# Optimization experiments

Hardware: AMD Instinct MI355X
Metric: run time of the kernel (lower is better)

Reference implementation:

```python
import jax, jax.numpy as jnp
import numpy as np

H = 128          # hidden_dim
EPS = 1e-5       # BatchNorm eps


def _mean_aggr(h_src, src_idx, dst_idx, num_dst):
    # scatter-mean of h_src rows (gathered by src_idx) onto dst nodes
    msgs = h_src[src_idx]                                   # [E, H] gather
    s = jax.ops.segment_sum(msgs, dst_idx, num_segments=num_dst)
    c = jax.ops.segment_sum(jnp.ones((dst_idx.shape[0],), h_src.dtype),
                            dst_idx, num_segments=num_dst)
    return s / jnp.maximum(c, 1.0)[:, None]


def _bn_eval(h, g, b, m, v):
    return (h - m) * jax.lax.rsqrt(v + EPS) * g + b


def setup_inputs() -> dict:
    key = jax.random.key(0)
    ks = jax.random.split(key, 32)
    Nu, Nr, E, Din, ED = 100000, 100000, 500000, 32, 16
    d = {}
    d['x_user'] = jax.random.normal(ks[0], (Nu, Din), jnp.float32)
    d['x_recipient'] = jax.random.normal(ks[1], (Nr, Din), jnp.float32)
    d['edge_attr'] = jax.random.normal(ks[2], (E, ED), jnp.float32)
    d['edge_index_ut'] = jax.random.randint(ks[3], (2, E), 0, Nr)  # user->recipient
    d['edge_index_ru'] = jax.random.randint(ks[4], (2, E), 0, Nu)  # recipient->user
    sc = 0.05
    # input projections (Linear: y = x @ W + b, W stored [in, out])
    d['proj_uW'] = jax.random.normal(ks[5], (Din, H), jnp.float32) * sc
    d['proj_ub'] = jnp.zeros((H,), jnp.float32)
    d['proj_rW'] = jax.random.normal(ks[6], (Din, H), jnp.float32) * sc
    d['proj_rb'] = jnp.zeros((H,), jnp.float32)
    # SAGEConv params: [num_layers=2, num_edge_types=2, ...]
    d['sage_Wl'] = jax.random.normal(ks[7], (2, 2, H, H), jnp.float32) * sc
    d['sage_bl'] = jnp.zeros((2, 2, H), jnp.float32)
    d['sage_Wr'] = jax.random.normal(ks[8], (2, 2, H, H), jnp.float32) * sc
    # BatchNorm (eval): [num_layers=2, num_node_types=2 (0=user,1=recipient), H]
    d['bn_g'] = jnp.ones((2, 2, H), jnp.float32)
    d['bn_b'] = jnp.zeros((2, 2, H), jnp.float32)
    d['bn_m'] = jax.random.normal(ks[9], (2, 2, H), jnp.float32) * 0.01
    d['bn_v'] = jnp.ones((2, 2, H), jnp.float32)
    # EdgePredictor MLP: (2H + edge_dim) -> H -> H//2 -> 1
    din = 2 * H + ED
    d['ep_W1'] = jax.random.normal(ks[10], (din, H), jnp.float32) * sc
    d['ep_b1'] = jnp.zeros((H,), jnp.float32)
    d['ep_bng'] = jnp.ones((H,), jnp.float32)
    d['ep_bnb'] = jnp.zeros((H,), jnp.float32)
    d['ep_bnm'] = jax.random.normal(ks[11], (H,), jnp.float32) * 0.01
    d['ep_bnv'] = jnp.ones((H,), jnp.float32)
    d['ep_W2'] = jax.random.normal(ks[12], (H, H // 2), jnp.float32) * sc
    d['ep_b2'] = jnp.zeros((H // 2,), jnp.float32)
    d['ep_W3'] = jax.random.normal(ks[13], (H // 2, 1), jnp.float32) * sc
    d['ep_b3'] = jnp.zeros((1,), jnp.float32)
    return d


def reference(x_user, x_recipient, edge_attr, edge_index_ut, edge_index_ru,
              proj_uW, proj_ub, proj_rW, proj_rb,
              sage_Wl, sage_bl, sage_Wr,
              bn_g, bn_b, bn_m, bn_v,
              ep_W1, ep_b1, ep_bng, ep_bnb, ep_bnm, ep_bnv,
              ep_W2, ep_b2, ep_W3, ep_b3):
    Nu = x_user.shape[0]
    Nr = x_recipient.shape[0]
    # input projections
    h_u = x_user @ proj_uW + proj_ub        # [Nu, H]
    h_r = x_recipient @ proj_rW + proj_rb   # [Nr, H]

    for i in range(2):  # num_layers
        # edge type 0: user -> recipient (SAGE mean aggr + root)
        agg_r = _mean_aggr(h_u, edge_index_ut[0], edge_index_ut[1], Nr)
        new_r = agg_r @ sage_Wl[i, 0] + sage_bl[i, 0] + h_r @ sage_Wr[i, 0]
        # edge type 1: recipient -> user
        agg_u = _mean_aggr(h_r, edge_index_ru[0], edge_index_ru[1], Nu)
        new_u = agg_u @ sage_Wl[i, 1] + sage_bl[i, 1] + h_u @ sage_Wr[i, 1]
        # BN (eval) + ReLU (dropout inactive) + residual
        new_u = jax.nn.relu(_bn_eval(new_u, bn_g[i, 0], bn_b[i, 0], bn_m[i, 0], bn_v[i, 0])) + h_u
        new_r = jax.nn.relu(_bn_eval(new_r, bn_g[i, 1], bn_b[i, 1], bn_m[i, 1], bn_v[i, 1])) + h_r
        h_u, h_r = new_u, new_r

    # edge predictor on target edge type (user -> recipient)
    src = h_u[edge_index_ut[0]]   # [E, H]
    dst = h_r[edge_index_ut[1]]   # [E, H]
    x = jnp.concatenate([src, dst, edge_attr], axis=1)  # [E, 2H+ED]
    h = jax.nn.relu(x @ ep_W1 + ep_b1)
    h = _bn_eval(h, ep_bng, ep_bnb, ep_bnm, ep_bnv)
    h = jax.nn.relu(h @ ep_W2 + ep_b2)
    out = jax.nn.sigmoid(h @ ep_W3 + ep_b3)
    return out.squeeze(-1)  # [E]
```

## Files before the change

kernel.cpp:

```cpp
#include <hip/hip_runtime.h>
#include <math.h>

#define H 128
#define BN_EPS 1e-5f

typedef __attribute__((ext_vector_type(8))) short bf16x8;
typedef __attribute__((ext_vector_type(4))) float f32x4;
typedef __attribute__((ext_vector_type(2))) float f32x2;

__device__ __forceinline__ unsigned short f2bf(float f) {
    unsigned int u = __float_as_uint(f);
    u += 0x7fffu + ((u >> 16) & 1u);
    return (unsigned short)(u >> 16);
}
__device__ __forceinline__ float bf2f(unsigned short s) {
    return __uint_as_float(((unsigned int)s) << 16);
}
__device__ __forceinline__ f32x4 mfma16(bf16x8 a, bf16x8 b, f32x4 c) {
    return __builtin_amdgcn_mfma_f32_16x16x32_bf16(a, b, c, 0, 0, 0);
}
__device__ __forceinline__ unsigned char f2fp8(float f) {
    int p = __builtin_amdgcn_cvt_pk_fp8_f32(f, f, 0, false);
    return (unsigned char)(p & 0xff);
}

__device__ __forceinline__ void wfrag_one(const float* __restrict__ src,
                                          unsigned short* __restrict__ dst,
                                          int K, int N, int idx) {
    int l = idx & 63;
    int rest = idx >> 6;
    int ntn = N >> 4;
    int nt = rest % ntn;
    int kc = rest / ntn;
    int n = nt * 16 + (l & 15);
    int k0 = kc * 32 + (l >> 4) * 8;
    bf16x8 v;
    #pragma unroll
    for (int j = 0; j < 8; ++j) {
        int k = k0 + j;
        v[j] = (short)((k < K) ? f2bf(src[(size_t)k * N + n]) : 0);
    }
    *(bf16x8*)(dst + (size_t)idx * 8) = v;
}

__global__ __launch_bounds__(256)
void wfrag_all(const float* __restrict__ W1, const float* __restrict__ W2,
               const float* __restrict__ pu, const float* __restrict__ pr,
               const float* __restrict__ Wl, const float* __restrict__ Wr,
               unsigned short* __restrict__ W1f, unsigned short* __restrict__ W2f,
               unsigned short* __restrict__ puf, unsigned short* __restrict__ prf,
               unsigned short* __restrict__ sageWf) {
    int bx = blockIdx.x;
    if (bx < 26) {
        int idx = bx * 256 + threadIdx.x;
        if (idx < 4608)      wfrag_one(W1, W1f, 272, 128, idx);
        else if (idx < 5632) wfrag_one(W2, W2f, 128, 64, idx - 4608);
        else if (idx < 6144) wfrag_one(pu, puf, 32, 128, idx - 5632);
        else if (idx < 6656) wfrag_one(pr, prf, 32, 128, idx - 6144);
    } else {
        int idx = (bx - 26) * 256 + threadIdx.x;
        int seg = idx >> 11;
        int sub = idx & 2047;
        int lt = seg >> 1;
        int half = seg & 1;
        const float* src = (half ? Wr : Wl) + (size_t)lt * H * H;
        unsigned short* dst = sageWf + (size_t)lt * 32768 + half * 16384;
        wfrag_one(src, dst, 128, 128, sub);
    }
}

__device__ __forceinline__ int swz_of(int col) {
    int kc = col >> 5;
    int q = (col >> 3) & 3;
    int j = col & 7;
    return q * 32 + kc * 8 + j;
}

__global__ __launch_bounds__(256)
void proj_kernel(const float* __restrict__ xu, const float* __restrict__ xr,
                 const unsigned short* __restrict__ puf, const float* __restrict__ bu,
                 const unsigned short* __restrict__ prf, const float* __restrict__ br,
                 unsigned short* __restrict__ hub, unsigned short* __restrict__ hrb,
                 unsigned char* __restrict__ h8u, unsigned char* __restrict__ h8r,
                 int Nu, int Nr, int nbu) {
    int bx = blockIdx.x;
    const float* x; const unsigned short* Wf; const float* bias;
    unsigned short* hb; unsigned char* h8; int N; int row0;
    if (bx < nbu) { x = xu; Wf = puf; bias = bu; hb = hub; h8 = h8u; N = Nu; row0 = bx * 64; }
    else          { x = xr; Wf = prf; bias = br; hb = hrb; h8 = h8r; N = Nr; row0 = (bx - nbu) * 64; }

    int tid = threadIdx.x, l = tid & 63, w = tid >> 6, l15 = l & 15, quad = l >> 4;
    int arow = row0 + w * 16 + l15;

    bf16x8 a = {0, 0, 0, 0, 0, 0, 0, 0};
    if (arow < N) {
        const float* xp = x + (size_t)arow * 32 + quad * 8;
        float4 v0 = *(const float4*)xp;
        float4 v1 = *(const float4*)(xp + 4);
        a[0] = (short)f2bf(v0.x); a[1] = (short)f2bf(v0.y);
        a[2] = (short)f2bf(v0.z); a[3] = (short)f2bf(v0.w);
        a[4] = (short)f2bf(v1.x); a[5] = (short)f2bf(v1.y);
        a[6] = (short)f2bf(v1.z); a[7] = (short)f2bf(v1.w);
    }
    f32x4 acc[8];
    #pragma unroll
    for (int nt = 0; nt < 8; ++nt) {
        bf16x8 b = *(const bf16x8*)(Wf + (size_t)(nt * 64 + l) * 8);
        acc[nt] = mfma16(a, b, (f32x4){0.f, 0.f, 0.f, 0.f});
    }
    #pragma unroll
    for (int reg = 0; reg < 4; ++reg) {
        int row = row0 + w * 16 + quad * 4 + reg;
        if (row < N) {
            #pragma unroll
            for (int nt = 0; nt < 8; ++nt) {
                int col = nt * 16 + l15;
                float v = acc[nt][reg] + bias[col];
                hb[(size_t)row * H + col] = f2bf(v);
                h8[(size_t)row * H + swz_of(col)] = f2fp8(v);
            }
        }
    }
}

__global__ __launch_bounds__(256)
void hist_kernel(const int* __restrict__ dstR, const int* __restrict__ dstU,
                 int* __restrict__ degR, int* __restrict__ degU, int E, int EB) {
    int bx = blockIdx.x;
    const int* dst = (bx < EB) ? dstR : dstU;
    int* deg = (bx < EB) ? degR : degU;
    int e = ((bx < EB) ? bx : bx - EB) * 256 + threadIdx.x;
    if (e < E) atomicAdd(&deg[dst[e]], 1);
}

__global__ __launch_bounds__(256)
void scan1_kernel(const int* __restrict__ degR, const int* __restrict__ degU,
                  int* __restrict__ partR, int* __restrict__ partU, int Nr, int Nu, int NBr) {
    int bx = blockIdx.x;
    const int* deg = (bx < NBr) ? degR : degU;
    int* part = (bx < NBr) ? partR : partU;
    int lb = (bx < NBr) ? bx : bx - NBr;
    int N = (bx < NBr) ? Nr : Nu;
    __shared__ int s[256];
    int t = threadIdx.x;
    int i = lb * 256 + t;
    s[t] = (i < N) ? deg[i] : 0;
    __syncthreads();
    for (int o = 128; o > 0; o >>= 1) {
        if (t < o) s[t] += s[t + o];
        __syncthreads();
    }
    if (t == 0) part[lb] = s[0];
}

__global__ __launch_bounds__(256)
void scan3_kernel(const int* __restrict__ degR, const int* __restrict__ degU,
                  const int* __restrict__ partR, const int* __restrict__ partU,
                  int* __restrict__ offR, int* __restrict__ offU, int Nr, int Nu, int NBr) {
    int bx = blockIdx.x;
    const int* deg = (bx < NBr) ? degR : degU;
    const int* part = (bx < NBr) ? partR : partU;
    int* off = (bx < NBr) ? offR : offU;
    int lb = (bx < NBr) ? bx : bx - NBr;
    int N = (bx < NBr) ? Nr : Nu;
    __shared__ int s[256];
    __shared__ int ps[256];
    int t = threadIdx.x;

    int pv = 0;
    if (t < lb) pv += part[t];
    if (t + 256 < lb) pv += part[t + 256];
    ps[t] = pv;
    __syncthreads();
    for (int o = 128; o > 0; o >>= 1) {
        if (t < o) ps[t] += ps[t + o];
        __syncthreads();
    }
    int pref = ps[0];

    int i = lb * 256 + t;
    int v = (i < N) ? deg[i] : 0;
    s[t] = v;
    __syncthreads();
    for (int o = 1; o < 256; o <<= 1) {
        int x = (t >= o) ? s[t - o] : 0;
        __syncthreads();
        s[t] += x;
        __syncthreads();
    }
    if (i < N) off[i] = pref + s[t] - v;
    if (i == N - 1) off[N] = pref + s[t];
}

__global__ __launch_bounds__(256)
void fill_kernel(const int* __restrict__ srcR, const int* __restrict__ dstR,
                 const int* __restrict__ srcU, const int* __restrict__ dstU,
                 const int* __restrict__ offR, const int* __restrict__ offU,
                 int* __restrict__ degR, int* __restrict__ degU,
                 int* __restrict__ eidR, int* __restrict__ eidU,
                 int* __restrict__ epermR, int* __restrict__ epdstR,
                 int E, int EB) {
    int bx = blockIdx.x;
    bool isR = bx < EB;
    const int* src = isR ? srcR : srcU;
    const int* dst = isR ? dstR : dstU;
    const int* off = isR ? offR : offU;
    int* deg = isR ? degR : degU;
    int* eid = isR ? eidR : eidU;
    int e = (isR ? bx : bx - EB) * 256 + threadIdx.x;
    if (e < E) {
        int d = dst[e];
        int p = off[d] + atomicSub(&deg[d], 1) - 1;
        eid[p] = src[e];
        if (isR) {
            epermR[p] = e;
            epdstR[p] = d;
        }
    }
}

__global__ __launch_bounds__(256)
void layer_kernel(const unsigned short* __restrict__ hu_o, const unsigned short* __restrict__ hr_o,
                  const unsigned char* __restrict__ h8u_o, const unsigned char* __restrict__ h8r_o,
                  unsigned short* __restrict__ hu_n, unsigned short* __restrict__ hr_n,
                  unsigned char* __restrict__ h8u_n, unsigned char* __restrict__ h8r_n,
                  const int* __restrict__ off_r, const int* __restrict__ eid_r,
                  const int* __restrict__ off_u, const int* __restrict__ eid_u,
                  int Nu, int Nr, int nbr,
                  const unsigned short* __restrict__ WfR, const float* __restrict__ blR,
                  const float* __restrict__ gR, const float* __restrict__ bR,
                  const float* __restrict__ mR, const float* __restrict__ vR,
                  const unsigned short* __restrict__ WfU, const float* __restrict__ blU,
                  const float* __restrict__ gU, const float* __restrict__ bU,
                  const float* __restrict__ mU, const float* __restrict__ vU) {
    int bx = blockIdx.x;
    const unsigned short* own; const unsigned char* g8; unsigned short* outp; unsigned char* out8;
    const int* off; const int* eid; const unsigned short* Wf;
    const float *bl, *bg, *bb, *bm, *bv;
    int N, row0;
    if (bx < nbr) {
        g8 = h8u_o; own = hr_o; outp = hr_n; out8 = h8r_n; off = off_r; eid = eid_r;
        Wf = WfR; bl = blR; bg = gR; bb = bR; bm = mR; bv = vR;
        N = Nr; row0 = bx * 64;
    } else {
        g8 = h8r_o; own = hu_o; outp = hu_n; out8 = h8u_n; off = off_u; eid = eid_u;
        Wf = WfU; bl = blU; bg = gU; bb = bU; bm = mU; bv = vU;
        N = Nu; row0 = (bx - nbr) * 64;
    }

    __shared__ float sc[128], sh[128], bias[128];
    __shared__ int perm[64];
    int tid = threadIdx.x;
    if (tid < 128) {
        float s = bg[tid] * rsqrtf(bv[tid] + BN_EPS);
        sc[tid] = s;
        sh[tid] = bb[tid] - bm[tid] * s;
        bias[tid] = bl[tid];
    }
    if (tid < 64) {
        int rr = row0 + tid;
        int dg = (rr < N) ? (off[rr + 1] - off[rr]) : 0;
        int key = (min(dg, 255) << 8) | tid;
        for (int k = 2; k <= 64; k <<= 1) {
            for (int j = k >> 1; j > 0; j >>= 1) {
                int p = __shfl_xor(key, j);
                bool keepmin = (((tid & j) == 0) == ((tid & k) == 0));
                key = keepmin ? (key < p ? key : p) : (key > p ? key : p);
            }
        }
        perm[tid] = key & 255;
    }
    __syncthreads();

    int l = tid & 63, w = tid >> 6, l15 = l & 15, quad = l >> 4;
    int rloc = perm[w * 16 + l15];
    int arow = row0 + rloc;
    bool rok = (arow < N);
    size_t rbase = (size_t)(rok ? arow : 0) * H;
    int s0 = rok ? off[arow] : 0;
    int s1 = rok ? off[arow + 1] : 0;

    bf16x8 ownfr[4];
    #pragma unroll
    for (int kc = 0; kc < 4; ++kc)
        ownfr[kc] = *(const bf16x8*)(own + rbase + kc * 32 + quad * 8);

    float ag[4][8];
    #pragma unroll
    for (int kc = 0; kc < 4; ++kc)
        #pragma unroll
        for (int j = 0; j < 8; ++j) ag[kc][j] = 0.0f;

    for (int i = s0; i < s1; ++i) {
        int s = eid[i];
        const uint4* rp = (const uint4*)(g8 + (size_t)s * H + quad * 32);
        uint4 w0 = rp[0];
        uint4 w1 = rp[1];
        #define ACC4(word, kc, jb) { \
            f32x2 lo_ = __builtin_amdgcn_cvt_pk_f32_fp8((int)(word), false); \
            f32x2 hi_ = __builtin_amdgcn_cvt_pk_f32_fp8((int)(word), true);  \
            ag[kc][jb + 0] += lo_[0]; ag[kc][jb + 1] += lo_[1]; \
            ag[kc][jb + 2] += hi_[0]; ag[kc][jb + 3] += hi_[1]; }
        ACC4(w0.x, 0, 0) ACC4(w0.y, 0, 4) ACC4(w0.z, 1, 0) ACC4(w0.w, 1, 4)
        ACC4(w1.x, 2, 0) ACC4(w1.y, 2, 4) ACC4(w1.z, 3, 0) ACC4(w1.w, 3, 4)
        #undef ACC4
    }
    float inv = (s1 > s0) ? 1.0f / (float)(s1 - s0) : 0.0f;

    f32x4 acc[8];
    #pragma unroll
    for (int nt = 0; nt < 8; ++nt) acc[nt] = (f32x4){0.f, 0.f, 0.f, 0.f};

    #pragma unroll
    for (int kc = 0; kc < 4; ++kc) {
        bf16x8 a;
        #pragma unroll
        for (int j = 0; j < 8; ++j) a[j] = (short)f2bf(ag[kc][j] * inv);
        #pragma unroll
        for (int nt = 0; nt < 8; ++nt) {
            bf16x8 b = *(const bf16x8*)(Wf + (size_t)((kc * 8 + nt) * 64 + l) * 8);
            acc[nt] = mfma16(a, b, acc[nt]);
        }
    }
    #pragma unroll
    for (int kc = 4; kc < 8; ++kc) {
        #pragma unroll
        for (int nt = 0; nt < 8; ++nt) {
            bf16x8 b = *(const bf16x8*)(Wf + (size_t)((kc * 8 + nt) * 64 + l) * 8);
            acc[nt] = mfma16(ownfr[kc - 4], b, acc[nt]);
        }
    }

    #pragma unroll
    for (int reg = 0; reg < 4; ++reg) {
        int crow = row0 + perm[w * 16 + quad * 4 + reg];
        if (crow < N) {
            #pragma unroll
            for (int nt = 0; nt < 8; ++nt) {
                int col = nt * 16 + l15;
                float g = acc[nt][reg] + bias[col];
                g = g * sc[col] + sh[col];
                float hv = bf2f(own[(size_t)crow * H + col]);
                float o = fmaxf(g, 0.0f) + hv;
                outp[(size_t)crow * H + col] = f2bf(o);
                out8[(size_t)crow * H + swz_of(col)] = f2fp8(o);
            }
        }
    }
}

__device__ __forceinline__ bf16x8 frag_fp8pair(unsigned int wa, unsigned int wb) {
    f32x2 a0 = __builtin_amdgcn_cvt_pk_f32_fp8((int)wa, false);
    f32x2 a1 = __builtin_amdgcn_cvt_pk_f32_fp8((int)wa, true);
    f32x2 b0 = __builtin_amdgcn_cvt_pk_f32_fp8((int)wb, false);
    f32x2 b1 = __builtin_amdgcn_cvt_pk_f32_fp8((int)wb, true);
    bf16x8 r;
    r[0] = (short)f2bf(a0[0]); r[1] = (short)f2bf(a0[1]);
    r[2] = (short)f2bf(a1[0]); r[3] = (short)f2bf(a1[1]);
    r[4] = (short)f2bf(b0[0]); r[5] = (short)f2bf(b0[1]);
    r[6] = (short)f2bf(b1[0]); r[7] = (short)f2bf(b1[1]);
    return r;
}

__global__ __launch_bounds__(256)
void ep_kernel(const unsigned char* __restrict__ h8u, const unsigned char* __restrict__ h8r,
               const float* __restrict__ ea,
               const int* __restrict__ slot_src, const int* __restrict__ slot_dst,
               const int* __restrict__ slot_eid,
               const unsigned short* __restrict__ W1f, const float* __restrict__ b1,
               const float* __restrict__ bng, const float* __restrict__ bnb,
               const float* __restrict__ bnm, const float* __restrict__ bnv,
               const unsigned short* __restrict__ W2f, const float* __restrict__ b2,
               const float* __restrict__ W3, const float* __restrict__ b3,
               float* __restrict__ out, int E) {
    __shared__ unsigned short h1s[64][136];
    __shared__ int se[64], de[64], pe[64];
    __shared__ float sc1[128], sh1[128], bi1[128];

    int tid = threadIdx.x;
    int p0 = blockIdx.x * 64;
    if (tid < 64) {
        int p = p0 + tid;
        bool v = (p < E);
        se[tid] = v ? slot_src[p] : 0;
        de[tid] = v ? slot_dst[p] : 0;
        pe[tid] = v ? slot_eid[p] : 0;
    }
    if (tid < 128) {
        float s = bng[tid] * rsqrtf(bnv[tid] + BN_EPS);
        sc1[tid] = s;
        sh1[tid] = bnb[tid] - bnm[tid] * s;
        bi1[tid] = b1[tid];
    }
    __syncthreads();

    int l = tid & 63, w = tid >> 6, l15 = l & 15, quad = l >> 4;
    int arow = w * 16 + l15;
    int eorig = pe[arow];
    bool ev = (p0 + arow < E);

    const uint4* sp = (const uint4*)(h8u + (size_t)se[arow] * H + quad * 32);
    const uint4* dp = (const uint4*)(h8r + (size_t)de[arow] * H + quad * 32);
    uint4 sw0 = sp[0], sw1 = sp[1];
    uint4 dw0 = dp[0], dw1 = dp[1];
    bf16x8 aea = {0, 0, 0, 0, 0, 0, 0, 0};
    if (quad < 2 && ev) {
        const float* p = ea + (size_t)eorig * 16 + quad * 8;
        float4 v0 = *(const float4*)p;
        float4 v1 = *(const float4*)(p + 4);
        aea[0] = (short)f2bf(v0.x); aea[1] = (short)f2bf(v0.y);
        aea[2] = (short)f2bf(v0.z); aea[3] = (short)f2bf(v0.w);
        aea[4] = (short)f2bf(v1.x); aea[5] = (short)f2bf(v1.y);
        aea[6] = (short)f2bf(v1.z); aea[7] = (short)f2bf(v1.w);
    }
    bf16x8 afr[9];
    afr[0] = frag_fp8pair(sw0.x, sw0.y);
    afr[1] = frag_fp8pair(sw0.z, sw0.w);
    afr[2] = frag_fp8pair(sw1.x, sw1.y);
    afr[3] = frag_fp8pair(sw1.z, sw1.w);
    afr[4] = frag_fp8pair(dw0.x, dw0.y);
    afr[5] = frag_fp8pair(dw0.z, dw0.w);
    afr[6] = frag_fp8pair(dw1.x, dw1.y);
    afr[7] = frag_fp8pair(dw1.z, dw1.w);
    afr[8] = aea;

    f32x4 acc[8];
    #pragma unroll
    for (int nt = 0; nt < 8; ++nt) acc[nt] = (f32x4){0.f, 0.f, 0.f, 0.f};

    #pragma unroll
    for (int kc = 0; kc < 9; ++kc) {
        #pragma unroll
        for (int nt = 0; nt < 8; ++nt) {
            bf16x8 b = *(const bf16x8*)(W1f + (size_t)((kc * 8 + nt) * 64 + l) * 8);
            acc[nt] = mfma16(afr[kc], b, acc[nt]);
        }
    }

    #pragma unroll
    for (int nt = 0; nt < 8; ++nt) {
        #pragma unroll
        for (int reg = 0; reg < 4; ++reg) {
            int row = w * 16 + quad * 4 + reg;
            int col = nt * 16 + l15;
            float z = acc[nt][reg] + bi1[col];
            z = fmaxf(z, 0.0f);
            z = z * sc1[col] + sh1[col];
            h1s[row][col] = f2bf(z);
        }
    }
    __syncthreads();

    f32x4 acc2[4];
    #pragma unroll
    for (int nt = 0; nt < 4; ++nt) acc2[nt] = (f32x4){0.f, 0.f, 0.f, 0.f};
    #pragma unroll
    for (int kc = 0; kc < 4; ++kc) {
        bf16x8 a2 = *(const bf16x8*)&h1s[w * 16 + l15][kc * 32 + quad * 8];
        #pragma unroll
        for (int nt = 0; nt < 4; ++nt) {
            bf16x8 b = *(const bf16x8*)(W2f + (size_t)((kc * 4 + nt) * 64 + l) * 8);
            acc2[nt] = mfma16(a2, b, acc2[nt]);
        }
    }

    float part[4] = {0.f, 0.f, 0.f, 0.f};
    #pragma unroll
    for (int nt = 0; nt < 4; ++nt) {
        int col = nt * 16 + l15;
        float w3v = W3[col];
        float b2v = b2[col];
        #pragma unroll
        for (int reg = 0; reg < 4; ++reg)
            part[reg] += fmaxf(acc2[nt][reg] + b2v, 0.0f) * w3v;
    }
    #pragma unroll
    for (int m = 1; m < 16; m <<= 1) {
        #pragma unroll
        for (int reg = 0; reg < 4; ++reg)
            part[reg] += __shfl_xor(part[reg], m);
    }
    if (l15 < 4) {
        int row = w * 16 + quad * 4 + l15;
        if (p0 + row < E) {
            int eo = pe[row];
            out[eo] = 1.0f / (1.0f + expf(-(part[l15] + b3[0])));
        }
    }
}

extern "C" void kernel_launch(void* const* d_in, const int* in_sizes, int n_in,
                              void* d_out, int out_size, void* d_ws, size_t ws_size,
                              hipStream_t stream) {
    const float* x_u     = (const float*)d_in[0];
    const float* x_r     = (const float*)d_in[1];
    const float* eattr   = (const float*)d_in[2];
    const int*   ei_ut   = (const int*)d_in[3];
    const int*   ei_ru   = (const int*)d_in[4];
    const float* proj_uW = (const float*)d_in[5];
    const float* proj_ub = (const float*)d_in[6];
    const float* proj_rW = (const float*)d_in[7];
    const float* proj_rb = (const float*)d_in[8];
    const float* sage_Wl = (const float*)d_in[9];
    const float* sage_bl = (const float*)d_in[10];
    const float* sage_Wr = (const float*)d_in[11];
    const float* bn_g    = (const float*)d_in[12];
    const float* bn_b    = (const float*)d_in[13];
    const float* bn_m    = (const float*)d_in[14];
    const float* bn_v    = (const float*)d_in[15];
    const float* ep_W1   = (const float*)d_in[16];
    const float* ep_b1   = (const float*)d_in[17];
    const float* ep_bng  = (const float*)d_in[18];
    const float* ep_bnb  = (const float*)d_in[19];
    const float* ep_bnm  = (const float*)d_in[20];
    const float* ep_bnv  = (const float*)d_in[21];
    const float* ep_W2   = (const float*)d_in[22];
    const float* ep_b2   = (const float*)d_in[23];
    const float* ep_W3   = (const float*)d_in[24];
    const float* ep_b3   = (const float*)d_in[25];

    int Nu = in_sizes[0] / 32;
    int Nr = in_sizes[1] / 32;
    int E  = in_sizes[3] / 2;

    unsigned short* us = (unsigned short*)d_ws;
    unsigned short* h0_u = us;   us += (size_t)Nu * H;
    unsigned short* h0_r = us;   us += (size_t)Nr * H;
    unsigned short* h1_u = us;   us += (size_t)Nu * H;
    unsigned short* h1_r = us;   us += (size_t)Nr * H;
    unsigned short* W1f  = us;   us += 36864;
    unsigned short* W2f  = us;   us += 8192;
    unsigned short* puf  = us;   us += 4096;
    unsigned short* prf  = us;   us += 4096;
    unsigned short* sageWf = us; us += 131072;
    unsigned char* f80_u = (unsigned char*)us;
    unsigned char* f80_r = f80_u + (size_t)Nu * H;
    unsigned char* f81_u = f80_r + (size_t)Nr * H;
    unsigned char* f81_r = f81_u + (size_t)Nu * H;
    int* ip     = (int*)(f81_r + (size_t)Nr * H);
    int* off_r  = ip;  ip += Nr + 1;
    int* off_u  = ip;  ip += Nu + 1;
    int* deg_r  = ip;  ip += Nr;
    int* deg_u  = ip;  ip += Nu;
    int* eid_r  = ip;  ip += E;
    int* eid_u  = ip;  ip += E;
    int* eperm_r = ip; ip += E;
    int* epdst_r = ip; ip += E;
    int* part_r = ip;  ip += 512;
    int* part_u = ip;  ip += 512;

    const int* ut_src = ei_ut;
    const int* ut_dst = ei_ut + E;
    const int* ru_src = ei_ru;
    const int* ru_dst = ei_ru + E;

    int EB  = (E + 255) / 256;
    int NBr = (Nr + 255) / 256;
    int NBu = (Nu + 255) / 256;

    wfrag_all<<<90, 256, 0, stream>>>(ep_W1, ep_W2, proj_uW, proj_rW,
                                      sage_Wl, sage_Wr,
                                      W1f, W2f, puf, prf, sageWf);

    hipMemsetAsync(deg_r, 0, (size_t)(Nr + Nu) * sizeof(int), stream);
    hist_kernel<<<2 * EB, 256, 0, stream>>>(ut_dst, ru_dst, deg_r, deg_u, E, EB);
    scan1_kernel<<<NBr + NBu, 256, 0, stream>>>(deg_r, deg_u, part_r, part_u, Nr, Nu, NBr);
    scan3_kernel<<<NBr + NBu, 256, 0, stream>>>(deg_r, deg_u, part_r, part_u,
                                                off_r, off_u, Nr, Nu, NBr);
    fill_kernel<<<2 * EB, 256, 0, stream>>>(ut_src, ut_dst, ru_src, ru_dst,
                                            off_r, off_u, deg_r, deg_u,
                                            eid_r, eid_u, eperm_r, epdst_r, E, EB);

    int nbu = (Nu + 63) / 64, nbr = (Nr + 63) / 64;
    proj_kernel<<<nbu + nbr, 256, 0, stream>>>(x_u, x_r, puf, proj_ub, prf, proj_rb,
                                               h0_u, h0_r, f80_u, f80_r, Nu, Nr, nbu);

    for (int layer = 0; layer < 2; ++layer) {
        const unsigned short* iu = (layer == 0) ? h0_u : h1_u;
        const unsigned short* ir = (layer == 0) ? h0_r : h1_r;
        const unsigned char* i8u = (layer == 0) ? f80_u : f81_u;
        const unsigned char* i8r = (layer == 0) ? f80_r : f81_r;
        unsigned short* ou = (layer == 0) ? h1_u : h0_u;
        unsigned short* orr = (layer == 0) ? h1_r : h0_r;
        unsigned char* o8u = (layer == 0) ? f81_u : f80_u;
        unsigned char* o8r = (layer == 0) ? f81_r : f80_r;

        const unsigned short* Wf0 = sageWf + ((size_t)layer * 2 + 0) * 32768;
        const unsigned short* Wf1 = sageWf + ((size_t)layer * 2 + 1) * 32768;
        const float* bl0 = sage_bl + ((size_t)layer * 2 + 0) * H;
        const float* bl1 = sage_bl + ((size_t)layer * 2 + 1) * H;
        const float* g0 = bn_g + ((size_t)layer * 2 + 0) * H;
        const float* b0 = bn_b + ((size_t)layer * 2 + 0) * H;
        const float* m0 = bn_m + ((size_t)layer * 2 + 0) * H;
        const float* v0 = bn_v + ((size_t)layer * 2 + 0) * H;
        const float* g1 = bn_g + ((size_t)layer * 2 + 1) * H;
        const float* b1 = bn_b + ((size_t)layer * 2 + 1) * H;
        const float* m1 = bn_m + ((size_t)layer * 2 + 1) * H;
        const float* v1 = bn_v + ((size_t)layer * 2 + 1) * H;

        layer_kernel<<<nbr + nbu, 256, 0, stream>>>(
            iu, ir, i8u, i8r, ou, orr, o8u, o8r,
            off_r, eid_r, off_u, eid_u,
            Nu, Nr, nbr,
            Wf0, bl0, g1, b1, m1, v1,
            Wf1, bl1, g0, b0, m0, v0);
    }

    ep_kernel<<<(E + 63) / 64, 256, 0, stream>>>(f80_u, f80_r, eattr,
                                                 eid_r, epdst_r, eperm_r,
                                                 W1f, ep_b1,
                                                 ep_bng, ep_bnb, ep_bnm, ep_bnv,
                                                 W2f, ep_b2, ep_W3, ep_b3,
                                                 (float*)d_out, E);
}
```

Baseline: 550.4 us.

## Stage edge-predictor MLP weights into LDS with double-buffered async global loads

The edge-predictor kernel previously had every wave read W1 and W2 MFMA fragments straight from global memory. Now the four waves of a block share the work of copying W1 fragments into a double-buffered LDS area with global_load_lds, prefetching the next K-chunk while the current one is used. W2 fragments are staged into LDS the same way before the second GEMM. The aim is to cut redundant global and L2 traffic across waves, at the cost of a __syncthreads per K-chunk and more LDS per block, which may lower occupancy.

Measured after the change: 531.0 us. 3.5% less time.

```diff
diff --git a/kernel.cpp b/kernel.cpp
--- a/kernel.cpp
+++ b/kernel.cpp
@@ -22,6 +22,11 @@
 __device__ __forceinline__ unsigned char f2fp8(float f) {
     int p = __builtin_amdgcn_cvt_pk_fp8_f32(f, f, 0, false);
     return (unsigned char)(p & 0xff);
+}
+__device__ __forceinline__ void gl_lds16(const void* g, void* l) {
+    __builtin_amdgcn_global_load_lds(
+        (const __attribute__((address_space(1))) unsigned int*)g,
+        (__attribute__((address_space(3))) unsigned int*)l, 16, 0, 0);
 }
 
 __device__ __forceinline__ void wfrag_one(const float* __restrict__ src,
@@ -374,6 +379,7 @@
                const float* __restrict__ W3, const float* __restrict__ b3,
                float* __restrict__ out, int E) {
     __shared__ unsigned short h1s[64][136];
+    __shared__ __align__(16) unsigned short Bst[2][4096];
     __shared__ int se[64], de[64], pe[64];
     __shared__ float sc1[128], sh1[128], bi1[128];
 
@@ -398,6 +404,13 @@
     int arow = w * 16 + l15;
     int eorig = pe[arow];
     bool ev = (p0 + arow < E);
+
+    #define STAGE_W1(kc, buf) { \
+        int nt0 = w * 2; \
+        gl_lds16(W1f + (((size_t)(kc) * 8 + nt0) * 64 + l) * 8, &Bst[buf][nt0 * 512]); \
+        gl_lds16(W1f + (((size_t)(kc) * 8 + nt0 + 1) * 64 + l) * 8, &Bst[buf][(nt0 + 1) * 512]); }
+
+    STAGE_W1(0, 0);
 
     const uint4* sp = (const uint4*)(h8u + (size_t)se[arow] * H + quad * 32);
     const uint4* dp = (const uint4*)(h8r + (size_t)de[arow] * H + quad * 32);
@@ -428,12 +441,28 @@
     #pragma unroll
     for (int nt = 0; nt < 8; ++nt) acc[nt] = (f32x4){0.f, 0.f, 0.f, 0.f};
 
+    __syncthreads();
+
+    int buf = 0;
     #pragma unroll
     for (int kc = 0; kc < 9; ++kc) {
+        if (kc < 8) STAGE_W1(kc + 1, buf ^ 1);
         #pragma unroll
         for (int nt = 0; nt < 8; ++nt) {
-            bf16x8 b = *(const bf16x8*)(W1f + (size_t)((kc * 8 + nt) * 64 + l) * 8);
+            bf16x8 b = *(const bf16x8*)&Bst[buf][nt * 512 + l * 8];
             acc[nt] = mfma16(afr[kc], b, acc[nt]);
+        }
+        __syncthreads();
+        buf ^= 1;
+    }
+    #undef STAGE_W1
+
+    {
+        unsigned short* BstF = &Bst[0][0];
+        #pragma unroll
+        for (int j = 0; j < 4; ++j) {
+            int f = w * 4 + j;
+            gl_lds16(W2f + ((size_t)f * 64 + l) * 8, BstF + f * 512);
         }
     }
 
@@ -451,6 +480,7 @@
     }
     __syncthreads();
 
+    const unsigned short* BstF = &Bst[0][0];
     f32x4 acc2[4];
     #pragma unroll
     for (int nt = 0; nt < 4; ++nt) acc2[nt] = (f32x4){0.f, 0.f, 0.f, 0.f};
@@ -459,7 +489,7 @@
         bf16x8 a2 = *(const bf16x8*)&h1s[w * 16 + l15][kc * 32 + quad * 8];
         #pragma unroll
         for (int nt = 0; nt < 4; ++nt) {
-            bf16x8 b = *(const bf16x8*)(W2f + (size_t)((kc * 4 + nt) * 64 + l) * 8);
+            bf16x8 b = *(const bf16x8*)(BstF + (size_t)((kc * 4 + nt) * 512) + l * 8);
             acc2[nt] = mfma16(a2, b, acc2[nt]);
         }
     }
```
